# Performance work log

Hardware: AMD Instinct MI355X
Metric: run time of the kernel (lower is better)

The kernel has to match this reference:

```python
import jax, jax.numpy as jnp
import numpy as np

BATCH, IN_F, OUT_F = 1024, 512, 512
GRID_SIZE, SPLINE_ORDER = 32, 3
P_DEACTIVATE = 0.1


def b_splines(x, grid, k):
    """x: (n, in), grid: (in, G+2k+1) -> bases (n, in, G+k). Cox-de Boor recursion."""
    x = x[..., None]  # (n, in, 1)
    bases = ((x >= grid[:, :-1]) & (x < grid[:, 1:])).astype(x.dtype)
    for j in range(1, k + 1):
        left = (x - grid[:, : -(j + 1)]) / (grid[:, j:-1] - grid[:, : -(j + 1)])
        right = (grid[:, j + 1:] - x) / (grid[:, j + 1:] - grid[:, 1:-j])
        bases = left * bases[..., :-1] + right * bases[..., 1:]
    return bases


def setup_inputs() -> dict:
    key = jax.random.key(0)
    k1, k2, k3, k4, k5 = jax.random.split(key, 5)
    # uniform extended grid over [-1, 1], same for every input feature
    h = 2.0 / GRID_SIZE
    knots = np.arange(-SPLINE_ORDER, GRID_SIZE + SPLINE_ORDER + 1, dtype=np.float32) * h - 1.0
    grid = jnp.asarray(np.tile(knots, (IN_F, 1)))  # (in, G+2k+1)
    return {
        "x": jax.random.normal(k1, (BATCH, IN_F), jnp.float32),
        "base_weight": jax.random.normal(k2, (OUT_F, IN_F), jnp.float32) * 0.05,
        "spline_weight": jax.random.normal(k3, (OUT_F, IN_F, GRID_SIZE + SPLINE_ORDER), jnp.float32) * 0.1,
        "spline_scaler": jax.random.normal(k4, (OUT_F, IN_F), jnp.float32),
        "grid": grid,
        "deactivate_mask": jax.random.bernoulli(k5, P_DEACTIVATE, (OUT_F, IN_F)),
    }


def reference(x, base_weight, spline_weight, spline_scaler, grid, deactivate_mask):
    k = SPLINE_ORDER
    weights = spline_weight * spline_scaler[..., None]  # scaled_spline_weight (o, i, c)
    # base path: F.linear(silu(x), base_weight)
    base_out = jax.nn.silu(x) @ base_weight.T  # (b, o)
    # spline path
    bases = b_splines(x, grid, k)  # (b, i, c)
    contrib = jnp.einsum('bic,oic->boi', bases, weights)  # (b, o, i)
    # linear fallback from spline values at grid endpoints
    gmin = grid[:, k].min()
    gmax = grid[:, -k - 1].max()
    ends_x = jnp.stack([gmin, gmax])[:, None] * jnp.ones((1, x.shape[1]), x.dtype)  # (2, i)
    y_ends = jnp.einsum('nic,oic->noi', b_splines(ends_x, grid, k), weights)  # (2, o, i)
    y_start, y_end = y_ends[0], y_ends[1]
    dx = gmax - gmin
    degenerate = jnp.abs(dx) < 1e-8
    a = jnp.where(degenerate, 0.0, (y_end - y_start) / jnp.where(degenerate, 1.0, dx))  # (o, i)
    b = y_start - a * gmin
    lin = a[None] * x[:, None, :] + b[None]  # (b, o, i)
    final = jnp.where(deactivate_mask[None], lin, contrib)
    return base_out + final.sum(axis=2)
```

## Files before the change

### kernel.cpp

```cpp
#include <hip/hip_runtime.h>
#include <hip/hip_bf16.h>


typedef unsigned short u16;
typedef unsigned int u32;
typedef unsigned long long u64;
typedef __attribute__((ext_vector_type(8))) short short8;
typedef __attribute__((ext_vector_type(4))) float floatx4;
typedef __attribute__((ext_vector_type(4))) unsigned int uintx4;

#define IN_F 512
#define OUT_F 512
#define BATCH 1024
#define K_SPLINE (IN_F * 36)
#define K_BASE_OFF K_SPLINE
#define K_LIN_OFF (K_SPLINE + IN_F)
#define K_TOT (K_SPLINE + 2 * IN_F)
#define SPLITS 32
#define MN (BATCH * OUT_F)

#define BARRIER_LGKM() asm volatile("s_waitcnt lgkmcnt(0)\n\ts_barrier" ::: "memory")

static __device__ inline u16 f2b(float f) {
  union { float f; u32 u; } v; v.f = f;
  u32 r = v.u + 0x7FFFu + ((v.u >> 16) & 1u);
  return (u16)(r >> 16);
}
static __device__ inline float b2f(u32 lo16) {
  union { u32 u; float f; } v; v.u = lo16 << 16; return v.f;
}

__global__ __launch_bounds__(256) void prep_kernel(
    const float* __restrict__ bw, const float* __restrict__ sw,
    const float* __restrict__ sc, const void* __restrict__ maskp,
    const float* __restrict__ x, u16* __restrict__ B,
    float* __restrict__ bias_part, u64* __restrict__ PB8) {
  __shared__ u64 lds64[1120 * 4];
  __shared__ int sflag;
  __shared__ float ws4[4];
  int blk = blockIdx.x, t = threadIdx.x;

  if (blk >= 1024) {
    int id = (blk - 1024) * 256 + t;
    float xv = x[id];
    int mc = (int)floorf((xv + 1.1875f) * 16.0f);
    float gm = (float)mc * 0.0625f - 1.1875f;
    if (xv < gm) { mc -= 1; gm -= 0.0625f; }
    else if (xv >= gm + 0.0625f) { mc += 1; gm += 0.0625f; }
    u32 lo, hi;
    if (mc >= 0 && mc <= 37) {
      float t_ = (xv - gm) * 16.0f;
      float t2 = t_ * t_, t3 = t2 * t_;
      float omt = 1.0f - t_;
      u16 r0 = f2b(omt * omt * omt * (1.0f / 6.0f));
      u16 r1 = f2b((3.0f * t3 - 6.0f * t2 + 4.0f) * (1.0f / 6.0f));
      u16 r2 = f2b((-3.0f * t3 + 3.0f * t2 + 3.0f * t_ + 1.0f) * (1.0f / 6.0f));
      lo = (u32)r0 | ((u32)r1 << 16);
      hi = (u32)r2 | ((u32)mc << 16);
    } else {
      lo = 0; hi = 0xFFFF0000u;
    }
    PB8[id] = (u64)lo | ((u64)hi << 32);
    return;
  }

  float* lds_f = (float*)lds64;
  u16* lds_u = (u16*)lds64;
  int id = blk * 256 + t;
  int o = id >> 9, i = id & 511;
  int i0 = (blk & 1) * 256;

  const float* swb = sw + ((size_t)o * 512 + i0) * 35;
#pragma unroll
  for (int j = 0; j < 35; ++j) lds_f[j * 256 + t] = swb[j * 256 + t];

  const u32* mw = (const u32*)maskp;
  if (t == 0) sflag = 0;
  __syncthreads();
  if (t < 64) {
    u32 w2 = mw[blk * 64 + t];
    if ((w2 & 0xFFFFFF00u) && w2 != 0x3F800000u) atomicOr(&sflag, 1);
  }
  __syncthreads();
  int fl = sflag;
  if (!(fl & 1)) {
    u32 w1 = mw[blk * 256 + t];
    if (w1 == 0x3F800000u) atomicOr(&sflag, 2);
  }
  __syncthreads();
  fl = sflag;
  bool mk;
  if (fl & 1)      mk = ((const unsigned char*)maskp)[id] != 0;
  else if (fl & 2) mk = ((const float*)maskp)[id] != 0.0f;
  else             mk = ((const int*)maskp)[id] != 0;

  float s = sc[id];
  float w[35];
#pragma unroll
  for (int c = 0; c < 35; ++c) w[c] = lds_f[t * 35 + c] * s;
  __syncthreads();

  float ys = (w[0] + 4.0f * w[1] + w[2]) * (1.0f / 6.0f);
  float ye = (w[32] + 4.0f * w[33] + w[34]) * (1.0f / 6.0f);
  float a = (ye - ys) * 0.5f;
  float bl = ys + a;

#pragma unroll
  for (int c = 0; c < 35; ++c) lds_u[t * 36 + c] = f2b(mk ? 0.0f : w[c]);
  lds_u[t * 36 + 35] = 0;

  B[(size_t)o * K_TOT + K_BASE_OFF + i] = f2b(bw[id]);
  B[(size_t)o * K_TOT + K_LIN_OFF + i] = f2b(mk ? a : 0.0f);

  float v = mk ? bl : 0.0f;
#pragma unroll
  for (int off = 32; off >= 1; off >>= 1) v += __shfl_down(v, off);
  if ((t & 63) == 0) ws4[t >> 6] = v;
  __syncthreads();
  if (t == 0) bias_part[blk] = ws4[0] + ws4[1] + ws4[2] + ws4[3];

  u64* dst = (u64*)(B + (size_t)o * K_TOT + (size_t)i0 * 36);
#pragma unroll
  for (int j = 0; j < 9; ++j) dst[j * 256 + t] = lds64[j * 256 + t];
}

__global__ __launch_bounds__(256) void gemm_fused(const float* __restrict__ x,
                                                  const u64* __restrict__ PB8,
                                                  const u16* __restrict__ Bp,
                                                  u16* __restrict__ P) {
  __shared__ u16 As0[128 * 64 + 64];
  __shared__ u16 As1[128 * 64 + 64];

  int t = threadIdx.x;
  int id = blockIdx.x;
  int ks = id >> 5, tile = id & 31;
  int bm = tile >> 2, bn = tile & 3;
  int w = t >> 6, l = t & 63;
  int wm = w & 1, wn = w >> 1;
  int mr = l & 15, cq = l >> 4;

  floatx4 acc[4][4];
#pragma unroll
  for (int p = 0; p < 4; ++p)
#pragma unroll
    for (int q = 0; q < 4; ++q) acc[p][q] = (floatx4)0.0f;

  int nit = (ks < 16) ? 10 : 9;
  int k0s = (ks < 16) ? ks * 640 : 10240 + (ks - 16) * 576;

  const u16* Bgf = Bp + (size_t)(bn * 128 + wn * 64 + mr) * K_TOT + cq * 8;

  int rr_ = t >> 1, hf = t & 1;
  int rx7 = rr_ & 7;
  const u64* PBrow = PB8 + (size_t)(bm * 128 + rr_) * IN_F;

  int if_cur = 0; u64 e0 = 0, e1 = 0;

  auto loadB = [&](short8 (&dst)[8], int k0b) {
#pragma unroll
    for (int h = 0; h < 2; ++h)
#pragma unroll
      for (int tn = 0; tn < 4; ++tn)
        dst[h * 4 + tn] =
            *(const short8*)(Bgf + (size_t)(tn * 16) * K_TOT + k0b + h * 32);
  };

  auto buildA = [&](int kkb, u16* A) {
    int dummy = 128 * 64 + (t & 63);
    int k0b = k0s + kkb * 64;
    if (k0b < K_BASE_OFF) {
#pragma unroll
      for (int q = 0; q < 4; ++q) {
        int ch = hf * 4 + q;
        *(uintx4*)&A[rr_ * 64 + ((ch ^ rx7) << 3)] = (uintx4)0u;
      }
      int k0w = k0b + hf * 32;
      int i_last = (k0w + 31) / 36;
#pragma unroll
      for (int ii = 0; ii < 2; ++ii) {
        int i = if_cur + ii;
        if (i <= i_last) {
          u64 e = ii ? e1 : e0;
          u32 lo = (u32)e, hi = (u32)(e >> 32);
          int mc = (int)(hi >> 16);
          float f0 = b2f(lo & 0xFFFFu);
          float f1 = b2f(lo >> 16);
          float f2 = b2f(hi & 0xFFFFu);
          u16 bv[4] = {(u16)lo, (u16)(lo >> 16), (u16)hi, f2b(1.0f - f0 - f1 - f2)};
          int cb = i * 36 + mc - 3 - k0b;
#pragma unroll
          for (int j = 0; j < 4; ++j) {
            int c = cb + j;
            bool ok = ((u32)(c - hf * 32) < 32u) && ((u32)(mc - 3 + j) < 35u);
            int addr = ok ? (rr_ * 64 + (((c >> 3) ^ rx7) << 3) + (c & 7)) : dummy;
            A[addr] = bv[j];
          }
        }
      }
      int k0n = k0b + 64;
      if (k0n < K_BASE_OFF) {
        int if_n = (k0n + hf * 32) / 36;
        if_cur = if_n;
        e0 = PBrow[if_n];
        e1 = PBrow[if_n + 1];
      }
    } else {
      bool isBase = (k0b < K_LIN_OFF);
      int xb = isBase ? (k0b - K_BASE_OFF) : (k0b - K_LIN_OFF);
#pragma unroll
      for (int p = 0; p < 4; ++p) {
        int cid = t + 256 * p;
        int row = cid >> 3, ch = cid & 7;
        const float* xp = &x[(size_t)(bm * 128 + row) * IN_F + xb + ch * 8];
        floatx4 v0 = *(const floatx4*)xp;
        floatx4 v1 = *(const floatx4*)(xp + 4);
        float f[8] = {v0.x, v0.y, v0.z, v0.w, v1.x, v1.y, v1.z, v1.w};
        u16 r[8];
#pragma unroll
        for (int j = 0; j < 8; ++j) {
          float vv = f[j];
          if (isBase) vv = vv / (1.0f + __expf(-vv));
          r[j] = f2b(vv);
        }
        *(short8*)(A + row * 64 + ((ch ^ (row & 7)) << 3)) = *(short8*)r;
      }
    }
  };

  auto mfmaStep = [&](const u16* A, short8 (&bf)[8]) {
#pragma unroll
    for (int h = 0; h < 2; ++h) {
      short8 af[4];
      int c = h * 4 + cq;
#pragma unroll
      for (int tm = 0; tm < 4; ++tm) {
        int row = wm * 64 + tm * 16 + mr;
        af[tm] = *(const short8*)&A[row * 64 + ((c ^ (row & 7)) << 3)];
      }
#pragma unroll
      for (int tm = 0; tm < 4; ++tm)
#pragma unroll
        for (int tn = 0; tn < 4; ++tn)
          acc[tm][tn] = __builtin_amdgcn_mfma_f32_16x16x32_bf16(
              af[tm], bf[h * 4 + tn], acc[tm][tn], 0, 0, 0);
    }
  };

  short8 bA[8], bB[8];

  if (k0s < K_BASE_OFF) {
    if_cur = (k0s + hf * 32) / 36;
    e0 = PBrow[if_cur];
    e1 = PBrow[if_cur + 1];
  }
  loadB(bA, k0s);
  buildA(0, As0);
  BARRIER_LGKM();

  int k0 = k0s;
  for (int kk = 0; kk < nit; kk += 2) {
    if (kk + 1 < nit) { loadB(bB, k0 + 64); buildA(kk + 1, As1); }
    mfmaStep(As0, bA);
    BARRIER_LGKM();
    k0 += 64;
    if (kk + 1 >= nit) break;
    if (kk + 2 < nit) { loadB(bA, k0 + 64); buildA(kk + 2, As0); }
    mfmaStep(As1, bB);
    BARRIER_LGKM();
    k0 += 64;
  }

  u16* Pb = P + ((size_t)tile * SPLITS + ks) * 16384;
#pragma unroll
  for (int q = 0; q < 8; ++q) {
    int tm = q >> 1, tn0 = (q & 1) * 2;
    u16 r[8];
#pragma unroll
    for (int z = 0; z < 4; ++z) r[z] = f2b(acc[tm][tn0][z]);
#pragma unroll
    for (int z = 0; z < 4; ++z) r[4 + z] = f2b(acc[tm][tn0 + 1][z]);
    *(short8*)(Pb + q * 2048 + t * 8) = *(short8*)r;
  }
}

__global__ __launch_bounds__(256) void reduce_kernel(const u16* __restrict__ P,
                                                     const float* __restrict__ bias_part,
                                                     float* __restrict__ out) {
  int rid = blockIdx.x * 256 + threadIdx.x;
  int tile = rid >> 11;
  int rem = rid & 2047;
  int q = rem >> 8, t = rem & 255;
  const u16* base = P + (size_t)tile * SPLITS * 16384 + q * 2048 + t * 8;

  float s[8] = {0, 0, 0, 0, 0, 0, 0, 0};
#pragma unroll
  for (int ks = 0; ks < SPLITS; ++ks) {
    short8 v = *(const short8*)(base + (size_t)ks * 16384);
#pragma unroll
    for (int j = 0; j < 8; ++j) s[j] += b2f((u32)(u16)v[j]);
  }

  int w = t >> 6, l = t & 63;
  int wm = w & 1, wn = w >> 1;
  int bm = tile >> 2, bn = tile & 3;
  int row0 = bm * 128 + wm * 64 + ((l >> 4) << 2);
  int col0 = bn * 128 + wn * 64 + (l & 15);
  int tm = q >> 1, tn0 = (q & 1) * 2;
#pragma unroll
  for (int j = 0; j < 8; ++j) {
    int tn = tn0 + (j >> 2), rr = j & 3;
    int row = row0 + tm * 16 + rr;
    int col = col0 + tn * 16;
    float bsv = bias_part[2 * col] + bias_part[2 * col + 1];
    out[(size_t)row * OUT_F + col] = s[j] + bsv;
  }
}

extern "C" void kernel_launch(void* const* d_in, const int* in_sizes, int n_in,
                              void* d_out, int out_size, void* d_ws, size_t ws_size,
                              hipStream_t stream) {
  const float* x  = (const float*)d_in[0];
  const float* bw = (const float*)d_in[1];
  const float* sw = (const float*)d_in[2];
  const float* sc = (const float*)d_in[3];
  const void* mask = d_in[5];

  const size_t B_BYTES = (size_t)OUT_F * K_TOT * 2;
  const size_t BIAS_OFF = B_BYTES;
  const size_t PB_OFF = B_BYTES + 8192;
  const size_t PB_BYTES = (size_t)MN * 8;
  const size_t P_OFF = PB_OFF + PB_BYTES;

  char* wsb = (char*)d_ws;
  u16* Bpack = (u16*)wsb;
  float* bias_part = (float*)(wsb + BIAS_OFF);
  u64* PB8 = (u64*)(wsb + PB_OFF);
  u16* P = (u16*)(wsb + P_OFF);

  prep_kernel<<<3072, 256, 0, stream>>>(bw, sw, sc, mask, x, Bpack, bias_part, PB8);
  gemm_fused<<<1024, 256, 0, stream>>>(x, PB8, Bpack, P);
  reduce_kernel<<<256, 256, 0, stream>>>(P, bias_part, (float*)d_out);
}
```

Baseline: 161.0 us.

## Stage B tiles in LDS via direct global-to-LDS loads

```diff
diff --git a/kernel.cpp b/kernel.cpp
--- a/kernel.cpp
+++ b/kernel.cpp
@@ -19,6 +19,7 @@
 #define SPLITS 32
 #define MN (BATCH * OUT_F)
 
+#define BARRIER_BARE() asm volatile("s_barrier" ::: "memory")
 #define BARRIER_LGKM() asm volatile("s_waitcnt lgkmcnt(0)\n\ts_barrier" ::: "memory")
 
 static __device__ inline u16 f2b(float f) {
@@ -130,6 +131,8 @@
                                                   u16* __restrict__ P) {
   __shared__ u16 As0[128 * 64 + 64];
   __shared__ u16 As1[128 * 64 + 64];
+  __shared__ u16 Bs0[128 * 64];
+  __shared__ u16 Bs1[128 * 64];
 
   int t = threadIdx.x;
   int id = blockIdx.x;
@@ -148,7 +151,9 @@
   int nit = (ks < 16) ? 10 : 9;
   int k0s = (ks < 16) ? ks * 640 : 10240 + (ks - 16) * 576;
 
-  const u16* Bgf = Bp + (size_t)(bn * 128 + wn * 64 + mr) * K_TOT + cq * 8;
+  int ra = t >> 3;
+  int cg = (t & 7) ^ (ra & 7);
+  const u16* Bg = Bp + (size_t)(bn * 128 + ra) * K_TOT + k0s + cg * 8;
 
   int rr_ = t >> 1, hf = t & 1;
   int rx7 = rr_ & 7;
@@ -156,13 +161,14 @@
 
   int if_cur = 0; u64 e0 = 0, e1 = 0;
 
-  auto loadB = [&](short8 (&dst)[8], int k0b) {
-#pragma unroll
-    for (int h = 0; h < 2; ++h)
-#pragma unroll
-      for (int tn = 0; tn < 4; ++tn)
-        dst[h * 4 + tn] =
-            *(const short8*)(Bgf + (size_t)(tn * 16) * K_TOT + k0b + h * 32);
+  auto issueB = [&](u16* Bbuf, int kkb) {
+    const u16* src = Bg + kkb * 64;
+    u16* dst = Bbuf + t * 8;
+#pragma unroll
+    for (int p = 0; p < 4; ++p)
+      __builtin_amdgcn_global_load_lds(
+          (const __attribute__((address_space(1))) void*)(src + (size_t)p * 32 * K_TOT),
+          (__attribute__((address_space(3))) void*)(dst + p * 2048), 16, 0, 0);
   };
 
   auto buildA = [&](int kkb, u16* A) {
@@ -227,10 +233,10 @@
     }
   };
 
-  auto mfmaStep = [&](const u16* A, short8 (&bf)[8]) {
+  auto mfmaStep = [&](const u16* A, const u16* Bbuf) {
 #pragma unroll
     for (int h = 0; h < 2; ++h) {
-      short8 af[4];
+      short8 af[4], bf[4];
       int c = h * 4 + cq;
 #pragma unroll
       for (int tm = 0; tm < 4; ++tm) {
@@ -238,36 +244,49 @@
         af[tm] = *(const short8*)&A[row * 64 + ((c ^ (row & 7)) << 3)];
       }
 #pragma unroll
+      for (int tn = 0; tn < 4; ++tn) {
+        int row = wn * 64 + tn * 16 + mr;
+        bf[tn] = *(const short8*)&Bbuf[row * 64 + ((c ^ (row & 7)) << 3)];
+      }
+#pragma unroll
       for (int tm = 0; tm < 4; ++tm)
 #pragma unroll
         for (int tn = 0; tn < 4; ++tn)
           acc[tm][tn] = __builtin_amdgcn_mfma_f32_16x16x32_bf16(
-              af[tm], bf[h * 4 + tn], acc[tm][tn], 0, 0, 0);
+              af[tm], bf[h * 4 ? tn : tn], acc[tm][tn], 0, 0, 0);
     }
   };
-
-  short8 bA[8], bB[8];
 
   if (k0s < K_BASE_OFF) {
     if_cur = (k0s + hf * 32) / 36;
     e0 = PBrow[if_cur];
     e1 = PBrow[if_cur + 1];
   }
-  loadB(bA, k0s);
+  issueB(Bs0, 0);
   buildA(0, As0);
   BARRIER_LGKM();
 
-  int k0 = k0s;
   for (int kk = 0; kk < nit; kk += 2) {
-    if (kk + 1 < nit) { loadB(bB, k0 + 64); buildA(kk + 1, As1); }
-    mfmaStep(As0, bA);
+    if (kk + 1 < nit) {
+      issueB(Bs1, kk + 1);
+      buildA(kk + 1, As1);
+    } else {
+      asm volatile("s_waitcnt vmcnt(0)" ::: "memory");
+    }
+    BARRIER_BARE();
+    mfmaStep(As0, Bs0);
     BARRIER_LGKM();
-    k0 += 64;
     if (kk + 1 >= nit) break;
-    if (kk + 2 < nit) { loadB(bA, k0 + 64); buildA(kk + 2, As0); }
-    mfmaStep(As1, bB);
+
+    if (kk + 2 < nit) {
+      issueB(Bs0, kk + 2);
+      buildA(kk + 2, As0);
+    } else {
+      asm volatile("s_waitcnt vmcnt(0)" ::: "memory");
+    }
+    BARRIER_BARE();
+    mfmaStep(As1, Bs1);
     BARRIER_LGKM();
-    k0 += 64;
   }
 
   u16* Pb = P + ((size_t)tile * SPLITS + ks) * 16384;
```

Result: faster. 146.1 us (-9.3%).
